# Optimization experiments

Hardware: AMD Instinct MI355X
Metric: run time of the kernel (lower is better)

Reference implementation:

```python
import jax, jax.numpy as jnp
import numpy as np

B, L, K, D = 65536, 4, 1024, 512


def setup_inputs() -> dict:
    key = jax.random.key(0)
    k1, k2 = jax.random.split(key)
    z_e = jax.random.normal(k1, (B, D), dtype=jnp.float32)
    # torch init: uniform(-1/codebook_size, 1/codebook_size)
    codebooks = jax.random.uniform(k2, (L, K, D), dtype=jnp.float32,
                                   minval=-1.0 / K, maxval=1.0 / K)
    return {"z_e": z_e, "codebooks": codebooks}


def reference(z_e, codebooks):
    sg = jax.lax.stop_gradient

    def step(carry, cb):
        # carry: (residual [B,D], quantized_sum [B,D], vq_loss scalar); cb: [K,D]
        residual, qsum, loss = carry
        # squared euclidean distances [B,K]
        d2 = (jnp.sum(residual * residual, axis=1, keepdims=True)
              + jnp.sum(cb * cb, axis=1)
              - 2.0 * residual @ cb.T)
        idx = jnp.argmin(d2, axis=1)          # [B]
        q = cb[idx]                           # [B,D] gather
        loss = loss + jnp.mean((q - sg(residual)) ** 2) \
                    + jnp.mean((sg(q) - residual) ** 2)
        return (residual - q, qsum + q, loss), idx

    init = (z_e, jnp.zeros_like(z_e), jnp.float32(0.0))
    (residual, qsum, vq_loss), codes = jax.lax.scan(step, init, codebooks)
    # straight-through estimator
    z_q_st = z_e + sg(qsum - z_e)
    return z_q_st, codes, vq_loss
```

## Files before the change

### kernel.cpp

```cpp
#include <hip/hip_runtime.h>
#include <math.h>

#define NB 65536
#define ND 512
#define NK 1024
#define NL 4
#define THR 1e-3f

typedef __attribute__((ext_vector_type(8))) short short8;
typedef __attribute__((ext_vector_type(4))) short short4_t;
typedef __attribute__((ext_vector_type(4))) float floatx4;

__device__ inline unsigned short bf16_rne(float x) {
  unsigned int u = __float_as_uint(x);
  unsigned int r = u + 0x7FFFu + ((u >> 16) & 1u);
  return (unsigned short)(r >> 16);
}

__global__ void cn_kernel(const float* __restrict__ cb, float* __restrict__ cn) {
  const int code = blockIdx.x;
  const float* row = cb + (size_t)code * ND;
  const int t = threadIdx.x;
  const float x = row[t];
  const float y = row[t + 256];
  double s = (double)x * x + (double)y * y;
  for (int off = 32; off > 0; off >>= 1) s += __shfl_down(s, off);
  __shared__ double part[4];
  if ((t & 63) == 0) part[t >> 6] = s;
  __syncthreads();
  if (t == 0) cn[code] = (float)(part[0] + part[1] + part[2] + part[3]);
}

__global__ void split_kernel(const float* __restrict__ x, short* __restrict__ hi,
                             short* __restrict__ lo) {
  const size_t i = ((size_t)blockIdx.x * 256 + threadIdx.x) * 4;
  const float4 v = *(const float4*)(x + i);
  const float av[4] = {v.x, v.y, v.z, v.w};
  short4_t h, l;
#pragma unroll
  for (int j = 0; j < 4; ++j) {
    unsigned short hb = bf16_rne(av[j]);
    float hf = __uint_as_float((unsigned int)hb << 16);
    h[j] = (short)hb;
    l[j] = (short)bf16_rne(av[j] - hf);
  }
  *(short4_t*)(hi + i) = h;
  *(short4_t*)(lo + i) = l;
}

__global__ void rn_kernel(const float* __restrict__ x, float* __restrict__ rn,
                          short* __restrict__ rh, short* __restrict__ rl, int do_split) {
  const int t = threadIdx.x;
  const int row = blockIdx.x * 2 + (t >> 7);
  const int c = (t & 127) << 2;
  const size_t off = (size_t)row * ND + c;
  const float4 v = *(const float4*)(x + off);
  if (do_split) {
    const float av[4] = {v.x, v.y, v.z, v.w};
    short4_t h, l;
#pragma unroll
    for (int j = 0; j < 4; ++j) {
      unsigned short hb = bf16_rne(av[j]);
      float hf = __uint_as_float((unsigned int)hb << 16);
      h[j] = (short)hb;
      l[j] = (short)bf16_rne(av[j] - hf);
    }
    *(short4_t*)(rh + off) = h;
    *(short4_t*)(rl + off) = l;
  }
  double s = (double)v.x * v.x + (double)v.y * v.y + (double)v.z * v.z + (double)v.w * v.w;
  for (int off2 = 32; off2 > 0; off2 >>= 1) s += __shfl_down(s, off2);
  __shared__ double part[4];
  if ((t & 63) == 0) part[t >> 6] = s;
  __syncthreads();
  if ((t & 127) == 0) rn[row] = (float)(part[t >> 6] + part[(t >> 6) + 1]);
}

template <int MODE>
__global__ __launch_bounds__(512, 2)
void argmin_mfma(const float* __restrict__ res,
                 const short* __restrict__ rh,
                 const short* __restrict__ rl,
                 const float* __restrict__ cb,
                 const short* __restrict__ cbh,
                 const short* __restrict__ cbl,
                 const float* __restrict__ rn,
                 const float* __restrict__ cn,
                 unsigned int* __restrict__ cnt,
                 unsigned int* __restrict__ cand) {
  __shared__ short A_hi[128][40];
  __shared__ short A_lo[128][40];
  __shared__ short B_hi[256][40];
  __shared__ short B_lo[256][40];
  __shared__ float minbuf[128][4];

  const int t = threadIdx.x;
  const int lane = t & 63;
  const int w = t >> 6;
  const int wr = w >> 2;
  const int wc = w & 3;
  const int q = lane >> 4;
  const int col16 = lane & 15;
  const int rowbase = (blockIdx.x >> 1) * 128;
  const int cbase = (blockIdx.x & 1) * 512;

  const int sa_row = t >> 2, sa_k = (t & 3) * 8;
  const int sb_row = t >> 1, sb_k = (t & 1) * 16;

  for (int nc = 0; nc < 2; ++nc) {
    floatx4 acc[4][4];
#pragma unroll
    for (int i = 0; i < 4; ++i)
#pragma unroll
      for (int j = 0; j < 4; ++j) acc[i][j] = (floatx4){0.f, 0.f, 0.f, 0.f};

    float4 fa0, fa1, fb[4];
    short8 pah, pal, pbh0, pbh1, pbl0, pbl1;
    {
      if constexpr (MODE == 2) {
        const size_t aoff = (size_t)(rowbase + sa_row) * ND + sa_k;
        pah = *(const short8*)(rh + aoff);
        pal = *(const short8*)(rl + aoff);
      } else {
        const float* ap = res + (size_t)(rowbase + sa_row) * ND + sa_k;
        fa0 = *(const float4*)(ap);
        fa1 = *(const float4*)(ap + 4);
      }
      if constexpr (MODE >= 1) {
        const size_t boff = (size_t)(cbase + nc * 256 + sb_row) * ND + sb_k;
        pbh0 = *(const short8*)(cbh + boff);
        pbh1 = *(const short8*)(cbh + boff + 8);
        pbl0 = *(const short8*)(cbl + boff);
        pbl1 = *(const short8*)(cbl + boff + 8);
      } else {
        const float* bp = cb + (size_t)(cbase + nc * 256 + sb_row) * ND + sb_k;
#pragma unroll
        for (int j = 0; j < 4; ++j) fb[j] = *(const float4*)(bp + 4 * j);
      }
    }

    for (int kc = 0; kc < 16; ++kc) {
      __syncthreads();
      if constexpr (MODE == 2) {
        *(short8*)&A_hi[sa_row][sa_k] = pah;
        *(short8*)&A_lo[sa_row][sa_k] = pal;
      } else {
        float av[8] = {fa0.x, fa0.y, fa0.z, fa0.w, fa1.x, fa1.y, fa1.z, fa1.w};
        short8 h, l;
#pragma unroll
        for (int j = 0; j < 8; ++j) {
          unsigned short hb = bf16_rne(av[j]);
          float hf = __uint_as_float((unsigned int)hb << 16);
          h[j] = (short)hb;
          l[j] = (short)bf16_rne(av[j] - hf);
        }
        *(short8*)&A_hi[sa_row][sa_k] = h;
        *(short8*)&A_lo[sa_row][sa_k] = l;
      }
      if constexpr (MODE >= 1) {
        *(short8*)&B_hi[sb_row][sb_k] = pbh0;
        *(short8*)&B_hi[sb_row][sb_k + 8] = pbh1;
        *(short8*)&B_lo[sb_row][sb_k] = pbl0;
        *(short8*)&B_lo[sb_row][sb_k + 8] = pbl1;
      } else {
        float bv[16];
#pragma unroll
        for (int j = 0; j < 4; ++j) {
          bv[4 * j + 0] = fb[j].x; bv[4 * j + 1] = fb[j].y;
          bv[4 * j + 2] = fb[j].z; bv[4 * j + 3] = fb[j].w;
        }
        short8 h0, l0, h1, l1;
#pragma unroll
        for (int j = 0; j < 8; ++j) {
          unsigned short hb = bf16_rne(bv[j]);
          float hf = __uint_as_float((unsigned int)hb << 16);
          h0[j] = (short)hb;
          l0[j] = (short)bf16_rne(bv[j] - hf);
          unsigned short hb1 = bf16_rne(bv[j + 8]);
          float hf1 = __uint_as_float((unsigned int)hb1 << 16);
          h1[j] = (short)hb1;
          l1[j] = (short)bf16_rne(bv[j + 8] - hf1);
        }
        *(short8*)&B_hi[sb_row][sb_k] = h0;
        *(short8*)&B_lo[sb_row][sb_k] = l0;
        *(short8*)&B_hi[sb_row][sb_k + 8] = h1;
        *(short8*)&B_lo[sb_row][sb_k + 8] = l1;
      }
      __syncthreads();
      if (kc + 1 < 16) {
        if constexpr (MODE == 2) {
          const size_t aoff = (size_t)(rowbase + sa_row) * ND + (kc + 1) * 32 + sa_k;
          pah = *(const short8*)(rh + aoff);
          pal = *(const short8*)(rl + aoff);
        } else {
          const float* ap = res + (size_t)(rowbase + sa_row) * ND + (kc + 1) * 32 + sa_k;
          fa0 = *(const float4*)(ap);
          fa1 = *(const float4*)(ap + 4);
        }
        if constexpr (MODE >= 1) {
          const size_t boff =
              (size_t)(cbase + nc * 256 + sb_row) * ND + (kc + 1) * 32 + sb_k;
          pbh0 = *(const short8*)(cbh + boff);
          pbh1 = *(const short8*)(cbh + boff + 8);
          pbl0 = *(const short8*)(cbl + boff);
          pbl1 = *(const short8*)(cbl + boff + 8);
        } else {
          const float* bp =
              cb + (size_t)(cbase + nc * 256 + sb_row) * ND + (kc + 1) * 32 + sb_k;
#pragma unroll
          for (int j = 0; j < 4; ++j) fb[j] = *(const float4*)(bp + 4 * j);
        }
      }
      short8 ahi[4], alo[4], bhi[4], blo[4];
#pragma unroll
      for (int ti = 0; ti < 4; ++ti) {
        const int m = wr * 64 + ti * 16 + col16;
        ahi[ti] = *(short8*)&A_hi[m][q * 8];
        alo[ti] = *(short8*)&A_lo[m][q * 8];
      }
#pragma unroll
      for (int tj = 0; tj < 4; ++tj) {
        const int n = wc * 64 + tj * 16 + col16;
        bhi[tj] = *(short8*)&B_hi[n][q * 8];
        blo[tj] = *(short8*)&B_lo[n][q * 8];
      }
#pragma unroll
      for (int ti = 0; ti < 4; ++ti)
#pragma unroll
        for (int tj = 0; tj < 4; ++tj) {
          acc[ti][tj] = __builtin_amdgcn_mfma_f32_16x16x32_bf16(ahi[ti], bhi[tj], acc[ti][tj], 0, 0, 0);
          acc[ti][tj] = __builtin_amdgcn_mfma_f32_16x16x32_bf16(alo[ti], bhi[tj], acc[ti][tj], 0, 0, 0);
          acc[ti][tj] = __builtin_amdgcn_mfma_f32_16x16x32_bf16(ahi[ti], blo[tj], acc[ti][tj], 0, 0, 0);
        }
    }

    float rnv[16], cnv[4];
#pragma unroll
    for (int ti = 0; ti < 4; ++ti)
#pragma unroll
      for (int v = 0; v < 4; ++v)
        rnv[ti * 4 + v] = rn[rowbase + wr * 64 + ti * 16 + q * 4 + v];
#pragma unroll
    for (int tj = 0; tj < 4; ++tj)
      cnv[tj] = cn[cbase + nc * 256 + wc * 64 + tj * 16 + col16];

    float rm[16];
#pragma unroll
    for (int ti = 0; ti < 4; ++ti)
#pragma unroll
      for (int v = 0; v < 4; ++v) {
        float m0 = INFINITY;
#pragma unroll
        for (int tj = 0; tj < 4; ++tj) {
          const float d2 = (rnv[ti * 4 + v] + cnv[tj]) - 2.0f * acc[ti][tj][v];
          m0 = fminf(m0, d2);
        }
        rm[ti * 4 + v] = m0;
      }
#pragma unroll
    for (int mask = 1; mask < 16; mask <<= 1)
#pragma unroll
      for (int i = 0; i < 16; ++i) rm[i] = fminf(rm[i], __shfl_xor(rm[i], mask));
    if (col16 == 0) {
#pragma unroll
      for (int ti = 0; ti < 4; ++ti)
#pragma unroll
        for (int v = 0; v < 4; ++v)
          minbuf[wr * 64 + ti * 16 + q * 4 + v][wc] = rm[ti * 4 + v];
    }
    __syncthreads();
    if (t < 128)
      minbuf[t][0] = fminf(fminf(minbuf[t][0], minbuf[t][1]), fminf(minbuf[t][2], minbuf[t][3]));
    __syncthreads();
#pragma unroll
    for (int ti = 0; ti < 4; ++ti)
#pragma unroll
      for (int v = 0; v < 4; ++v) {
        const int grow = rowbase + wr * 64 + ti * 16 + q * 4 + v;
        const float thrv = minbuf[wr * 64 + ti * 16 + q * 4 + v][0] + THR;
#pragma unroll
        for (int tj = 0; tj < 4; ++tj) {
          const float d2 = (rnv[ti * 4 + v] + cnv[tj]) - 2.0f * acc[ti][tj][v];
          if (d2 <= thrv) {
            const unsigned int gcol = cbase + nc * 256 + wc * 64 + tj * 16 + col16;
            const unsigned int slot = atomicAdd(&cnt[grow], 1u);
            if (slot < 16) cand[(size_t)grow * 16 + slot] = gcol;
          }
        }
      }
    __syncthreads();
  }
}

__global__ __launch_bounds__(256)
void recheck_kernel(const float* __restrict__ res, const float* __restrict__ cb,
                    const float* __restrict__ rn, const float* __restrict__ cn,
                    const unsigned int* __restrict__ cnt,
                    const unsigned int* __restrict__ cand,
                    int* __restrict__ idx) {
  const int t = threadIdx.x;
  const int lane = t & 63;
  const int slot = lane & 3;
  const int row = blockIdx.x * 64 + (t >> 2);
  const int wavebase = blockIdx.x * 64 + (t >> 6) * 16;
  const unsigned int c = cnt[row];
  const float* rp = res + (size_t)row * ND;
  const float rnr = rn[row];

  if (c <= 16) {
    float bestv = INFINITY;
    int bestk = 0x7fffffff;
    for (unsigned int s = slot; s < c; s += 4) {
      const int k = (int)cand[(size_t)row * 16 + s];
      const float* cp = cb + (size_t)k * ND;
      float acc = 0.f;
#pragma unroll 8
      for (int d = 0; d < ND; d += 4) {
        const float4 rv = *(const float4*)(rp + d);
        const float4 cv = *(const float4*)(cp + d);
        acc = fmaf(rv.x, cv.x, acc);
        acc = fmaf(rv.y, cv.y, acc);
        acc = fmaf(rv.z, cv.z, acc);
        acc = fmaf(rv.w, cv.w, acc);
      }
      const float d2 = (rnr + cn[k]) - 2.0f * acc;
      if (d2 < bestv || (d2 == bestv && k < bestk)) { bestv = d2; bestk = k; }
    }
#pragma unroll
    for (int off = 1; off < 4; off <<= 1) {
      const float ov = __shfl_xor(bestv, off);
      const int ok = __shfl_xor(bestk, off);
      if (ov < bestv || (ov == bestv && ok < bestk)) { bestv = ov; bestk = ok; }
    }
    if (slot == 0) idx[row] = bestk;
  }

  unsigned long long ovf = __ballot(slot == 0 && c > 16);
  while (ovf) {
    const int src = (int)__ffsll(ovf) - 1;
    ovf &= ovf - 1;
    const int orow = wavebase + (src >> 2);
    const float* orp = res + (size_t)orow * ND;
    const float ornr = rn[orow];
    float bv = INFINITY;
    int bk = 0x7fffffff;
    for (int kk = 0; kk < NK; kk += 64) {
      const int k = kk + lane;
      const float* cp = cb + (size_t)k * ND;
      float acc = 0.f;
      for (int d = 0; d < ND; d += 4) {
        const float4 rv = *(const float4*)(orp + d);
        const float4 cv = *(const float4*)(cp + d);
        acc = fmaf(rv.x, cv.x, acc);
        acc = fmaf(rv.y, cv.y, acc);
        acc = fmaf(rv.z, cv.z, acc);
        acc = fmaf(rv.w, cv.w, acc);
      }
      const float d2 = (ornr + cn[k]) - 2.0f * acc;
      if (d2 < bv || (d2 == bv && k < bk)) { bv = d2; bk = k; }
    }
    for (int off = 32; off > 0; off >>= 1) {
      const float ov = __shfl_down(bv, off);
      const int ok = __shfl_down(bk, off);
      if (ov < bv || (ov == bv && ok < bk)) { bv = ov; bk = ok; }
    }
    if (lane == 0) idx[orow] = bk;
  }
}

__global__ void update_kernel(const float* __restrict__ res_in,
                              const float* __restrict__ cb,
                              const int* __restrict__ idx,
                              float* __restrict__ res_out,
                              float* __restrict__ codes_out,
                              float* __restrict__ rn_out,
                              double* __restrict__ lacc,
                              short* __restrict__ rh, short* __restrict__ rl,
                              int do_split) {
  const int t = threadIdx.x;
  const int row = blockIdx.x * 2 + (t >> 7);
  const int c = (t & 127) << 2;
  const int k = idx[row];
  const size_t off = (size_t)row * ND + c;
  const float4 r = *(const float4*)(res_in + off);
  const float4 q = *(const float4*)(cb + (size_t)k * ND + c);
  float4 nr;
  nr.x = r.x - q.x; nr.y = r.y - q.y; nr.z = r.z - q.z; nr.w = r.w - q.w;
  *(float4*)(res_out + off) = nr;
  if (do_split) {
    const float av[4] = {nr.x, nr.y, nr.z, nr.w};
    short4_t h, l;
#pragma unroll
    for (int j = 0; j < 4; ++j) {
      unsigned short hb = bf16_rne(av[j]);
      float hf = __uint_as_float((unsigned int)hb << 16);
      h[j] = (short)hb;
      l[j] = (short)bf16_rne(av[j] - hf);
    }
    *(short4_t*)(rh + off) = h;
    *(short4_t*)(rl + off) = l;
  }
  if (c == 0) codes_out[row] = (float)k;
  double s = (double)nr.x * nr.x + (double)nr.y * nr.y +
             (double)nr.z * nr.z + (double)nr.w * nr.w;
  for (int off2 = 32; off2 > 0; off2 >>= 1) s += __shfl_down(s, off2);
  __shared__ double part[4];
  if ((t & 63) == 0) part[t >> 6] = s;
  __syncthreads();
  if ((t & 127) == 0) rn_out[row] = (float)(part[t >> 6] + part[(t >> 6) + 1]);
  if (t == 0) atomicAdd(&lacc[blockIdx.x & 511], part[0] + part[1] + part[2] + part[3]);
}

__global__ void loss_reduce(const double* __restrict__ lacc, float* __restrict__ out) {
  const int t = threadIdx.x;
  double s = 0.0;
  for (int i = t; i < NL * 512; i += 256) s += lacc[i];
  for (int off = 32; off > 0; off >>= 1) s += __shfl_down(s, off);
  __shared__ double part[4];
  if ((t & 63) == 0) part[t >> 6] = s;
  __syncthreads();
  if (t == 0)
    out[(size_t)NB * ND + (size_t)NL * NB] =
        (float)(2.0 * (part[0] + part[1] + part[2] + part[3]) / ((double)NB * (double)ND));
}

__global__ void final_kernel(const float* __restrict__ z_e,
                             const float* __restrict__ cbs,
                             float* __restrict__ out) {
  const size_t gid = (size_t)blockIdx.x * 256 + threadIdx.x;
  const int row = (int)(gid >> 7);
  const int c = ((int)gid & 127) << 2;
  const float* codes = out + (size_t)NB * ND;
  const int k0 = (int)codes[0 * NB + row];
  const int k1 = (int)codes[1 * NB + row];
  const int k2 = (int)codes[2 * NB + row];
  const int k3 = (int)codes[3 * NB + row];
  const float4 q0 = *(const float4*)(cbs + ((size_t)0 * NK + k0) * ND + c);
  const float4 q1 = *(const float4*)(cbs + ((size_t)1 * NK + k1) * ND + c);
  const float4 q2 = *(const float4*)(cbs + ((size_t)2 * NK + k2) * ND + c);
  const float4 q3 = *(const float4*)(cbs + ((size_t)3 * NK + k3) * ND + c);
  const float4 z = *(const float4*)(z_e + (size_t)row * ND + c);
  float4 qs, o;
  qs.x = ((q0.x + q1.x) + q2.x) + q3.x;
  qs.y = ((q0.y + q1.y) + q2.y) + q3.y;
  qs.z = ((q0.z + q1.z) + q2.z) + q3.z;
  qs.w = ((q0.w + q1.w) + q2.w) + q3.w;
  o.x = z.x + (qs.x - z.x);
  o.y = z.y + (qs.y - z.y);
  o.z = z.z + (qs.z - z.z);
  o.w = z.w + (qs.w - z.w);
  *(float4*)(out + (size_t)row * ND + c) = o;
}

extern "C" void kernel_launch(void* const* d_in, const int* in_sizes, int n_in,
                              void* d_out, int out_size, void* d_ws, size_t ws_size,
                              hipStream_t stream) {
  const float* z_e = (const float*)d_in[0];
  const float* cbs = (const float*)d_in[1];
  float* out = (float*)d_out;
  char* ws = (char*)d_ws;

  const size_t OFF_RN   = 16384;
  const size_t OFF_CN   = OFF_RN + 262144;
  const size_t OFF_CNT  = OFF_CN + 16384;
  const size_t OFF_CAND = OFF_CNT + 262144;
  const size_t OFF_IDX  = OFF_CAND + 4194304;
  const size_t OFF_CBH  = OFF_IDX + 262144;
  const size_t OFF_CBL  = OFF_CBH + (size_t)NL * NK * ND * 2;
  const size_t OFF_RH   = OFF_CBL + (size_t)NL * NK * ND * 2;
  const size_t OFF_RL   = OFF_RH + (size_t)NB * ND * 2;
  const size_t WS_MODE1 = OFF_RH;
  const size_t WS_MODE2 = OFF_RL + (size_t)NB * ND * 2;

  double* lacc = (double*)ws;
  float* rn = (float*)(ws + OFF_RN);
  float* cn = (float*)(ws + OFF_CN);
  unsigned int* cnt = (unsigned int*)(ws + OFF_CNT);
  unsigned int* cand = (unsigned int*)(ws + OFF_CAND);
  int* idx = (int*)(ws + OFF_IDX);
  short* cb_hi = (short*)(ws + OFF_CBH);
  short* cb_lo = (short*)(ws + OFF_CBL);
  short* res_hi = (short*)(ws + OFF_RH);
  short* res_lo = (short*)(ws + OFF_RL);

  int mode = 0;
  if (ws_size >= WS_MODE2) mode = 2;
  else if (ws_size >= WS_MODE1) mode = 1;

  float* resb = out;
  float* codes = out + (size_t)NB * ND;

  hipMemsetAsync(lacc, 0, NL * 512 * sizeof(double), stream);
  cn_kernel<<<NL * NK, 256, 0, stream>>>(cbs, cn);
  if (mode >= 1)
    split_kernel<<<(NL * NK * ND) / 1024, 256, 0, stream>>>(cbs, cb_hi, cb_lo);
  rn_kernel<<<NB / 2, 256, 0, stream>>>(z_e, rn, res_hi, res_lo, mode == 2 ? 1 : 0);

  for (int l = 0; l < NL; ++l) {
    const float* rin = (l == 0) ? z_e : resb;
    const float* cbl_f = cbs + (size_t)l * NK * ND;
    const short* cblh = cb_hi + (size_t)l * NK * ND;
    const short* cbll = cb_lo + (size_t)l * NK * ND;
    hipMemsetAsync(cnt, 0, (size_t)NB * 4, stream);
    if (mode == 2)
      argmin_mfma<2><<<(NB / 128) * 2, 512, 0, stream>>>(
          rin, res_hi, res_lo, cbl_f, cblh, cbll, rn, cn + l * NK, cnt, cand);
    else if (mode == 1)
      argmin_mfma<1><<<(NB / 128) * 2, 512, 0, stream>>>(
          rin, nullptr, nullptr, cbl_f, cblh, cbll, rn, cn + l * NK, cnt, cand);
    else
      argmin_mfma<0><<<(NB / 128) * 2, 512, 0, stream>>>(
          rin, nullptr, nullptr, cbl_f, nullptr, nullptr, rn, cn + l * NK, cnt, cand);
    recheck_kernel<<<NB / 64, 256, 0, stream>>>(rin, cbl_f, rn, cn + l * NK, cnt, cand, idx);
    update_kernel<<<NB / 2, 256, 0, stream>>>(
        rin, cbl_f, idx, resb, codes + (size_t)l * NB, rn, lacc + (size_t)l * 512,
        res_hi, res_lo, (mode == 2 && l < NL - 1) ? 1 : 0);
  }

  loss_reduce<<<1, 256, 0, stream>>>(lacc, out);
  final_kernel<<<(NB * (size_t)ND) / 4 / 256, 256, 0, stream>>>(z_e, cbs, out);
}
```

Measured before the change: 2.342 ms.

## Fuse recheck and update kernels, double-buffer argmin loads, skip last-layer residual write

```diff
diff --git a/kernel.cpp b/kernel.cpp
--- a/kernel.cpp
+++ b/kernel.cpp
@@ -114,103 +114,52 @@
 #pragma unroll
       for (int j = 0; j < 4; ++j) acc[i][j] = (floatx4){0.f, 0.f, 0.f, 0.f};
 
-    float4 fa0, fa1, fb[4];
-    short8 pah, pal, pbh0, pbh1, pbl0, pbl1;
-    {
+    auto load_chunk = [&](int kcc, short8& ah, short8& al, short8& bh0, short8& bh1,
+                          short8& bl0, short8& bl1) {
       if constexpr (MODE == 2) {
-        const size_t aoff = (size_t)(rowbase + sa_row) * ND + sa_k;
-        pah = *(const short8*)(rh + aoff);
-        pal = *(const short8*)(rl + aoff);
+        const size_t aoff = (size_t)(rowbase + sa_row) * ND + kcc * 32 + sa_k;
+        ah = *(const short8*)(rh + aoff);
+        al = *(const short8*)(rl + aoff);
+        const size_t boff = (size_t)(cbase + nc * 256 + sb_row) * ND + kcc * 32 + sb_k;
+        bh0 = *(const short8*)(cbh + boff);
+        bh1 = *(const short8*)(cbh + boff + 8);
+        bl0 = *(const short8*)(cbl + boff);
+        bl1 = *(const short8*)(cbl + boff + 8);
       } else {
-        const float* ap = res + (size_t)(rowbase + sa_row) * ND + sa_k;
-        fa0 = *(const float4*)(ap);
-        fa1 = *(const float4*)(ap + 4);
-      }
-      if constexpr (MODE >= 1) {
-        const size_t boff = (size_t)(cbase + nc * 256 + sb_row) * ND + sb_k;
-        pbh0 = *(const short8*)(cbh + boff);
-        pbh1 = *(const short8*)(cbh + boff + 8);
-        pbl0 = *(const short8*)(cbl + boff);
-        pbl1 = *(const short8*)(cbl + boff + 8);
-      } else {
-        const float* bp = cb + (size_t)(cbase + nc * 256 + sb_row) * ND + sb_k;
-#pragma unroll
-        for (int j = 0; j < 4; ++j) fb[j] = *(const float4*)(bp + 4 * j);
-      }
-    }
-
-    for (int kc = 0; kc < 16; ++kc) {
-      __syncthreads();
-      if constexpr (MODE == 2) {
-        *(short8*)&A_hi[sa_row][sa_k] = pah;
-        *(short8*)&A_lo[sa_row][sa_k] = pal;
-      } else {
-        float av[8] = {fa0.x, fa0.y, fa0.z, fa0.w, fa1.x, fa1.y, fa1.z, fa1.w};
-        short8 h, l;
+        const float* ap = res + (size_t)(rowbase + sa_row) * ND + kcc * 32 + sa_k;
+        const float4 fa0 = *(const float4*)(ap);
+        const float4 fa1 = *(const float4*)(ap + 4);
+        const float av[8] = {fa0.x, fa0.y, fa0.z, fa0.w, fa1.x, fa1.y, fa1.z, fa1.w};
 #pragma unroll
         for (int j = 0; j < 8; ++j) {
           unsigned short hb = bf16_rne(av[j]);
           float hf = __uint_as_float((unsigned int)hb << 16);
-          h[j] = (short)hb;
-          l[j] = (short)bf16_rne(av[j] - hf);
-        }
-        *(short8*)&A_hi[sa_row][sa_k] = h;
-        *(short8*)&A_lo[sa_row][sa_k] = l;
-      }
-      if constexpr (MODE >= 1) {
-        *(short8*)&B_hi[sb_row][sb_k] = pbh0;
-        *(short8*)&B_hi[sb_row][sb_k + 8] = pbh1;
-        *(short8*)&B_lo[sb_row][sb_k] = pbl0;
-        *(short8*)&B_lo[sb_row][sb_k + 8] = pbl1;
-      } else {
+          ah[j] = (short)hb;
+          al[j] = (short)bf16_rne(av[j] - hf);
+        }
+        const float* bp = cb + (size_t)(cbase + nc * 256 + sb_row) * ND + kcc * 32 + sb_k;
         float bv[16];
 #pragma unroll
         for (int j = 0; j < 4; ++j) {
-          bv[4 * j + 0] = fb[j].x; bv[4 * j + 1] = fb[j].y;
-          bv[4 * j + 2] = fb[j].z; bv[4 * j + 3] = fb[j].w;
-        }
-        short8 h0, l0, h1, l1;
+          const float4 fb = *(const float4*)(bp + 4 * j);
+          bv[4 * j + 0] = fb.x; bv[4 * j + 1] = fb.y;
+          bv[4 * j + 2] = fb.z; bv[4 * j + 3] = fb.w;
+        }
 #pragma unroll
         for (int j = 0; j < 8; ++j) {
           unsigned short hb = bf16_rne(bv[j]);
           float hf = __uint_as_float((unsigned int)hb << 16);
-          h0[j] = (short)hb;
-          l0[j] = (short)bf16_rne(bv[j] - hf);
+          bh0[j] = (short)hb;
+          bl0[j] = (short)bf16_rne(bv[j] - hf);
           unsigned short hb1 = bf16_rne(bv[j + 8]);
           float hf1 = __uint_as_float((unsigned int)hb1 << 16);
-          h1[j] = (short)hb1;
-          l1[j] = (short)bf16_rne(bv[j + 8] - hf1);
-        }
-        *(short8*)&B_hi[sb_row][sb_k] = h0;
-        *(short8*)&B_lo[sb_row][sb_k] = l0;
-        *(short8*)&B_hi[sb_row][sb_k + 8] = h1;
-        *(short8*)&B_lo[sb_row][sb_k + 8] = l1;
-      }
-      __syncthreads();
-      if (kc + 1 < 16) {
-        if constexpr (MODE == 2) {
-          const size_t aoff = (size_t)(rowbase + sa_row) * ND + (kc + 1) * 32 + sa_k;
-          pah = *(const short8*)(rh + aoff);
-          pal = *(const short8*)(rl + aoff);
-        } else {
-          const float* ap = res + (size_t)(rowbase + sa_row) * ND + (kc + 1) * 32 + sa_k;
-          fa0 = *(const float4*)(ap);
-          fa1 = *(const float4*)(ap + 4);
-        }
-        if constexpr (MODE >= 1) {
-          const size_t boff =
-              (size_t)(cbase + nc * 256 + sb_row) * ND + (kc + 1) * 32 + sb_k;
-          pbh0 = *(const short8*)(cbh + boff);
-          pbh1 = *(const short8*)(cbh + boff + 8);
-          pbl0 = *(const short8*)(cbl + boff);
-          pbl1 = *(const short8*)(cbl + boff + 8);
-        } else {
-          const float* bp =
-              cb + (size_t)(cbase + nc * 256 + sb_row) * ND + (kc + 1) * 32 + sb_k;
-#pragma unroll
-          for (int j = 0; j < 4; ++j) fb[j] = *(const float4*)(bp + 4 * j);
-        }
-      }
+          bh1[j] = (short)hb1;
+          bl1[j] = (short)bf16_rne(bv[j + 8] - hf1);
+        }
+      }
+    };
+
+    auto do_mfma = [&]() {
       short8 ahi[4], alo[4], bhi[4], blo[4];
 #pragma unroll
       for (int ti = 0; ti < 4; ++ti) {
@@ -232,6 +181,34 @@
           acc[ti][tj] = __builtin_amdgcn_mfma_f32_16x16x32_bf16(alo[ti], bhi[tj], acc[ti][tj], 0, 0, 0);
           acc[ti][tj] = __builtin_amdgcn_mfma_f32_16x16x32_bf16(ahi[ti], blo[tj], acc[ti][tj], 0, 0, 0);
         }
+    };
+
+    short8 a0h, a0l, b0h0, b0h1, b0l0, b0l1;
+    short8 a1h, a1l, b1h0, b1h1, b1l0, b1l1;
+    load_chunk(0, a0h, a0l, b0h0, b0h1, b0l0, b0l1);
+    load_chunk(1, a1h, a1l, b1h0, b1h1, b1l0, b1l1);
+
+    for (int kc = 0; kc < 16; kc += 2) {
+      __syncthreads();
+      *(short8*)&A_hi[sa_row][sa_k] = a0h;
+      *(short8*)&A_lo[sa_row][sa_k] = a0l;
+      *(short8*)&B_hi[sb_row][sb_k] = b0h0;
+      *(short8*)&B_hi[sb_row][sb_k + 8] = b0h1;
+      *(short8*)&B_lo[sb_row][sb_k] = b0l0;
+      *(short8*)&B_lo[sb_row][sb_k + 8] = b0l1;
+      __syncthreads();
+      if (kc + 2 < 16) load_chunk(kc + 2, a0h, a0l, b0h0, b0h1, b0l0, b0l1);
+      do_mfma();
+      __syncthreads();
+      *(short8*)&A_hi[sa_row][sa_k] = a1h;
+      *(short8*)&A_lo[sa_row][sa_k] = a1l;
+      *(short8*)&B_hi[sb_row][sb_k] = b1h0;
+      *(short8*)&B_hi[sb_row][sb_k + 8] = b1h1;
+      *(short8*)&B_lo[sb_row][sb_k] = b1l0;
+      *(short8*)&B_lo[sb_row][sb_k + 8] = b1l1;
+      __syncthreads();
+      if (kc + 3 < 16) load_chunk(kc + 3, a1h, a1l, b1h0, b1h1, b1l0, b1l1);
+      do_mfma();
     }
 
     float rnv[16], cnv[4];
@@ -293,23 +270,25 @@
 }
 
 __global__ __launch_bounds__(256)
-void recheck_kernel(const float* __restrict__ res, const float* __restrict__ cb,
+void resolve_kernel(const float* __restrict__ res_in, const float* __restrict__ cb,
                     const float* __restrict__ rn, const float* __restrict__ cn,
                     const unsigned int* __restrict__ cnt,
                     const unsigned int* __restrict__ cand,
-                    int* __restrict__ idx) {
+                    float* __restrict__ res_out, float* __restrict__ codes_out,
+                    float* __restrict__ rn_out, double* __restrict__ lacc,
+                    short* __restrict__ rh, short* __restrict__ rl, int flags) {
   const int t = threadIdx.x;
   const int lane = t & 63;
   const int slot = lane & 3;
   const int row = blockIdx.x * 64 + (t >> 2);
   const int wavebase = blockIdx.x * 64 + (t >> 6) * 16;
   const unsigned int c = cnt[row];
-  const float* rp = res + (size_t)row * ND;
+  const float* rp = res_in + (size_t)row * ND;
   const float rnr = rn[row];
 
+  float bestv = INFINITY;
+  int bestk = 0x7fffffff;
   if (c <= 16) {
-    float bestv = INFINITY;
-    int bestk = 0x7fffffff;
     for (unsigned int s = slot; s < c; s += 4) {
       const int k = (int)cand[(size_t)row * 16 + s];
       const float* cp = cb + (size_t)k * ND;
@@ -332,7 +311,6 @@
       const int ok = __shfl_xor(bestk, off);
       if (ov < bestv || (ov == bestv && ok < bestk)) { bestv = ov; bestk = ok; }
     }
-    if (slot == 0) idx[row] = bestk;
   }
 
   unsigned long long ovf = __ballot(slot == 0 && c > 16);
@@ -340,7 +318,7 @@
     const int src = (int)__ffsll(ovf) - 1;
     ovf &= ovf - 1;
     const int orow = wavebase + (src >> 2);
-    const float* orp = res + (size_t)orow * ND;
+    const float* orp = res_in + (size_t)orow * ND;
     const float ornr = rn[orow];
     float bv = INFINITY;
     int bk = 0x7fffffff;
@@ -364,50 +342,48 @@
       const int ok = __shfl_down(bk, off);
       if (ov < bv || (ov == bv && ok < bk)) { bv = ov; bk = ok; }
     }
-    if (lane == 0) idx[orow] = bk;
-  }
-}
-
-__global__ void update_kernel(const float* __restrict__ res_in,
-                              const float* __restrict__ cb,
-                              const int* __restrict__ idx,
-                              float* __restrict__ res_out,
-                              float* __restrict__ codes_out,
-                              float* __restrict__ rn_out,
-                              double* __restrict__ lacc,
-                              short* __restrict__ rh, short* __restrict__ rl,
-                              int do_split) {
-  const int t = threadIdx.x;
-  const int row = blockIdx.x * 2 + (t >> 7);
-  const int c = (t & 127) << 2;
-  const int k = idx[row];
-  const size_t off = (size_t)row * ND + c;
-  const float4 r = *(const float4*)(res_in + off);
-  const float4 q = *(const float4*)(cb + (size_t)k * ND + c);
-  float4 nr;
-  nr.x = r.x - q.x; nr.y = r.y - q.y; nr.z = r.z - q.z; nr.w = r.w - q.w;
-  *(float4*)(res_out + off) = nr;
-  if (do_split) {
-    const float av[4] = {nr.x, nr.y, nr.z, nr.w};
-    short4_t h, l;
-#pragma unroll
-    for (int j = 0; j < 4; ++j) {
-      unsigned short hb = bf16_rne(av[j]);
-      float hf = __uint_as_float((unsigned int)hb << 16);
-      h[j] = (short)hb;
-      l[j] = (short)bf16_rne(av[j] - hf);
-    }
-    *(short4_t*)(rh + off) = h;
-    *(short4_t*)(rl + off) = l;
-  }
-  if (c == 0) codes_out[row] = (float)k;
-  double s = (double)nr.x * nr.x + (double)nr.y * nr.y +
-             (double)nr.z * nr.z + (double)nr.w * nr.w;
-  for (int off2 = 32; off2 > 0; off2 >>= 1) s += __shfl_down(s, off2);
+    const int bkf = __shfl(bk, 0);
+    if ((lane >> 2) == (orow - wavebase)) bestk = bkf;
+  }
+
+  if (slot == 0) codes_out[row] = (float)bestk;
+
+  const float* qp = cb + (size_t)bestk * ND;
+  const int c0 = slot * 128;
+  double s = 0.0;
+#pragma unroll 4
+  for (int j = 0; j < 128; j += 4) {
+    const float4 r = *(const float4*)(rp + c0 + j);
+    const float4 qv = *(const float4*)(qp + c0 + j);
+    float4 nr;
+    nr.x = r.x - qv.x; nr.y = r.y - qv.y; nr.z = r.z - qv.z; nr.w = r.w - qv.w;
+    if (flags & 1) *(float4*)(res_out + (size_t)row * ND + c0 + j) = nr;
+    if (flags & 2) {
+      const float av[4] = {nr.x, nr.y, nr.z, nr.w};
+      short4_t h, l;
+#pragma unroll
+      for (int jj = 0; jj < 4; ++jj) {
+        unsigned short hb = bf16_rne(av[jj]);
+        float hf = __uint_as_float((unsigned int)hb << 16);
+        h[jj] = (short)hb;
+        l[jj] = (short)bf16_rne(av[jj] - hf);
+      }
+      *(short4_t*)(rh + (size_t)row * ND + c0 + j) = h;
+      *(short4_t*)(rl + (size_t)row * ND + c0 + j) = l;
+    }
+    s += (double)nr.x * nr.x + (double)nr.y * nr.y +
+         (double)nr.z * nr.z + (double)nr.w * nr.w;
+  }
+  s += __shfl_xor(s, 1);
+  s += __shfl_xor(s, 2);
+  if ((flags & 1) && slot == 0) rn_out[row] = (float)s;
+  s += __shfl_xor(s, 4);
+  s += __shfl_xor(s, 8);
+  s += __shfl_xor(s, 16);
+  s += __shfl_xor(s, 32);
   __shared__ double part[4];
-  if ((t & 63) == 0) part[t >> 6] = s;
+  if (lane == 0) part[t >> 6] = s;
   __syncthreads();
-  if ((t & 127) == 0) rn_out[row] = (float)(part[t >> 6] + part[(t >> 6) + 1]);
   if (t == 0) atomicAdd(&lacc[blockIdx.x & 511], part[0] + part[1] + part[2] + part[3]);
 }
 
@@ -469,7 +445,6 @@
   const size_t OFF_CBL  = OFF_CBH + (size_t)NL * NK * ND * 2;
   const size_t OFF_RH   = OFF_CBL + (size_t)NL * NK * ND * 2;
   const size_t OFF_RL   = OFF_RH + (size_t)NB * ND * 2;
-  const size_t WS_MODE1 = OFF_RH;
   const size_t WS_MODE2 = OFF_RL + (size_t)NB * ND * 2;
 
   double* lacc = (double*)ws;
@@ -477,22 +452,19 @@
   float* cn = (float*)(ws + OFF_CN);
   unsigned int* cnt = (unsigned int*)(ws + OFF_CNT);
   unsigned int* cand = (unsigned int*)(ws + OFF_CAND);
-  int* idx = (int*)(ws + OFF_IDX);
   short* cb_hi = (short*)(ws + OFF_CBH);
   short* cb_lo = (short*)(ws + OFF_CBL);
   short* res_hi = (short*)(ws + OFF_RH);
   short* res_lo = (short*)(ws + OFF_RL);
 
-  int mode = 0;
-  if (ws_size >= WS_MODE2) mode = 2;
-  else if (ws_size >= WS_MODE1) mode = 1;
+  const int mode = (ws_size >= WS_MODE2) ? 2 : 0;
 
   float* resb = out;
   float* codes = out + (size_t)NB * ND;
 
   hipMemsetAsync(lacc, 0, NL * 512 * sizeof(double), stream);
   cn_kernel<<<NL * NK, 256, 0, stream>>>(cbs, cn);
-  if (mode >= 1)
+  if (mode == 2)
     split_kernel<<<(NL * NK * ND) / 1024, 256, 0, stream>>>(cbs, cb_hi, cb_lo);
   rn_kernel<<<NB / 2, 256, 0, stream>>>(z_e, rn, res_hi, res_lo, mode == 2 ? 1 : 0);
 
@@ -504,17 +476,14 @@
     hipMemsetAsync(cnt, 0, (size_t)NB * 4, stream);
     if (mode == 2)
       argmin_mfma<2><<<(NB / 128) * 2, 512, 0, stream>>>(
-          rin, res_hi, res_lo, cbl_f, cblh, cbll, rn, cn + l * NK, cnt, cand);
-    else if (mode == 1)
-      argmin_mfma<1><<<(NB / 128) * 2, 512, 0, stream>>>(
-          rin, nullptr, nullptr, cbl_f, cblh, cbll, rn, cn + l * NK, cnt, cand);
+          nullptr, res_hi, res_lo, nullptr, cblh, cbll, rn, cn + l * NK, cnt, cand);
     else
       argmin_mfma<0><<<(NB / 128) * 2, 512, 0, stream>>>(
           rin, nullptr, nullptr, cbl_f, nullptr, nullptr, rn, cn + l * NK, cnt, cand);
-    recheck_kernel<<<NB / 64, 256, 0, stream>>>(rin, cbl_f, rn, cn + l * NK, cnt, cand, idx);
-    update_kernel<<<NB / 2, 256, 0, stream>>>(
-        rin, cbl_f, idx, resb, codes + (size_t)l * NB, rn, lacc + (size_t)l * 512,
-        res_hi, res_lo, (mode == 2 && l < NL - 1) ? 1 : 0);
+    const int flags = (l < NL - 1) ? (1 | (mode == 2 ? 2 : 0)) : 0;
+    resolve_kernel<<<NB / 64, 256, 0, stream>>>(
+        rin, cbl_f, rn, cn + l * NK, cnt, cand, resb, codes + (size_t)l * NB, rn,
+        lacc + (size_t)l * 512, res_hi, res_lo, flags);
   }
 
   loss_reduce<<<1, 256, 0, stream>>>(lacc, out);
```

Result: slower. 3.432 ms (+46.5%).
